# Kernel optimization log

Hardware: AMD Instinct MI355X
Metric: run time of the kernel (lower is better)

Reference implementation:

```python
import math
import jax, jax.numpy as jnp
import numpy as np

E_EDGES = 65536
N_NODES = 8192
MUL = 32
LAT = 128
COND = 32
# uuu tensor-product instructions (l1, l2, l_out) generated by the selection-rule loop
INSTR = [(0,0,0),(1,1,0),(2,2,0),
         (0,1,1),(1,0,1),(1,1,1),(1,2,1),(2,1,1),(2,2,1),
         (0,2,2),(1,1,2),(1,2,2),(2,0,2),(2,1,2),(2,2,2)]

# ---- real Wigner-3j (invariant 3-tensor) via null space of equivariance constraints ----
def _su2_J(l):
    m = np.arange(-l, l + 1)
    Jz = np.diag(m).astype(complex)
    d = 2 * l + 1
    Jp = np.zeros((d, d), complex)
    Jp[np.arange(1, d), np.arange(0, d - 1)] = np.sqrt((l - m[:-1]) * (l + m[:-1] + 1))
    Jm = Jp.conj().T
    return (Jp + Jm) / 2, (Jp - Jm) / 2j, Jz

def _q(l):
    q = np.zeros((2 * l + 1, 2 * l + 1), complex)
    for m in range(-l, 0):
        q[l + m, l + abs(m)] = 1 / np.sqrt(2)
        q[l + m, l - abs(m)] = -1j / np.sqrt(2)
    q[l, l] = 1.0
    for m in range(1, l + 1):
        q[l + m, l + abs(m)] = (-1) ** m / np.sqrt(2)
        q[l + m, l - abs(m)] = 1j * (-1) ** m / np.sqrt(2)
    return q

def _gen(l):
    q = _q(l)
    return [np.real(q.conj().T @ (-1j * J) @ q) for J in _su2_J(l)]

def _w3j(l1, l2, l3):
    G1, G2, G3 = _gen(l1), _gen(l2), _gen(l3)
    d1, d2, d3 = 2 * l1 + 1, 2 * l2 + 1, 2 * l3 + 1
    rows = []
    for a in range(3):
        rows.append(np.kron(np.kron(G1[a], np.eye(d2)), np.eye(d3))
                    + np.kron(np.kron(np.eye(d1), G2[a]), np.eye(d3))
                    + np.kron(np.kron(np.eye(d1), np.eye(d2)), G3[a]))
    _, _, vt = np.linalg.svd(np.concatenate(rows, 0))
    c = vt[-1]
    c = c / np.linalg.norm(c)
    c = c * np.sign(c[np.argmax(np.abs(c))])
    return c.reshape(d1, d2, d3).astype(np.float32)

W3J = {}
for _k in INSTR:
    if _k not in W3J:
        W3J[_k] = jnp.asarray(_w3j(*_k))

def _split9(x):
    # (E, MUL, 9) -> per-l blocks (widths 1,3,5)
    return (x[:, :, 0:1], x[:, :, 1:4], x[:, :, 4:9])

def _so3_ln(blocks, gamma, eps=1e-6):
    out = []
    for b, x in enumerate(blocks):
        if x.shape[-1] == 1:  # scalars: centered layernorm over channels
            mu = jnp.mean(x, axis=1, keepdims=True)
            var = jnp.mean((x - mu) ** 2, axis=1, keepdims=True)
            x = (x - mu) * jax.lax.rsqrt(var + eps)
        else:  # l>0: RMS over (channel, m), no centering (equivariance)
            ms = jnp.mean(x ** 2, axis=(1, 2), keepdims=True)
            x = x * jax.lax.rsqrt(ms + eps)
        out.append(x * gamma[b][None, :, None])
    return out

def _forward(scalar_latent, equiv_latent, edge_conditioning, update_coeff,
             W_env, b_env0, gamma_env, Wg_env, bg_env, gamma_tp,
             W1_s, b1_s, W2_s, b2_s, Weq0, beq0, Weq1, Weq2, Wg_eq, bg_eq,
             edge_index, active_edges):
    E = scalar_latent.shape[0]
    edge_center = edge_index[0]
    # env_eq: per-l SO3 linear (channel mixing), bias on l=0
    xb = _split9(equiv_latent)
    env = [jnp.einsum('eum,vu->evm', xb[l], W_env[l]) for l in range(3)]
    env[0] = env[0] + b_env0[None, :, None]
    gate_in = jnp.concatenate([scalar_latent, edge_conditioning], axis=-1)  # (E,160)
    g_env = 1.0 + 0.1 * jnp.tanh(gate_in @ Wg_env + bg_env[0])
    env_edges = jnp.concatenate(env, axis=-1) * g_env[:, None, None]
    # scatter-sum edges -> nodes, SO3 layernorm, gather back per edge
    env_nodes = jax.ops.segment_sum(env_edges, edge_center, num_segments=N_NODES)
    env_nodes = jnp.concatenate(_so3_ln(_split9(env_nodes), gamma_env), axis=-1)
    local = env_nodes[edge_center]  # (E, MUL, 9)
    # selection-rule-sparse tensor product, uuu, component-normalized
    x1b = _split9(equiv_latent)
    x2b = _split9(local)
    tp_blocks = [math.sqrt(2 * lo + 1) * jnp.einsum('ijk,eui,euj->euk', W3J[(l1, l2, lo)], x1b[l1], x2b[l2])
                 for (l1, l2, lo) in INSTR]
    tp_blocks = _so3_ln(tp_blocks, gamma_tp)
    # scalar (l=0) slices -> (E, 3*MUL)
    tp_scalars = jnp.concatenate(tp_blocks[0:3], axis=-1).reshape(E, -1)
    scalar_in = jnp.concatenate([tp_scalars, edge_conditioning], axis=-1)
    new_scalar = jax.nn.silu(scalar_in @ W1_s.T + b1_s) @ W2_s.T + b2_s  # (E, LAT)
    # equiv_update: SO3 linear tp_out_irreps -> equiv_latent_irreps
    x0 = tp_scalars  # (E, 3*MUL)
    out0 = (x0 @ Weq0.T + beq0)[:, :, None]                      # (E, MUL, 1)
    out1 = jnp.einsum('eum,vu->evm', jnp.concatenate(tp_blocks[3:9], axis=1), Weq1)   # (E, MUL, 3)
    out2 = jnp.einsum('eum,vu->evm', jnp.concatenate(tp_blocks[9:15], axis=1), Weq2)  # (E, MUL, 5)
    new_equiv = jnp.concatenate([out0, out1, out2], axis=-1)
    g_eq = 1.0 + 0.1 * jnp.tanh(gate_in @ Wg_eq + bg_eq[0])
    new_equiv = new_equiv * g_eq[:, None, None]
    # residual stream with update coefficient + index_add over active_edges
    c = update_coeff[0]
    co = jax.lax.rsqrt(c * c + 1.0)
    cn = c * co
    s_out = (co * scalar_latent).at[active_edges].add(cn * new_scalar)
    e_out = (co * equiv_latent).at[active_edges].add(cn * new_equiv)
    return s_out, e_out

def setup_inputs() -> dict:
    key = jax.random.key(0)
    ks = jax.random.split(key, 16)
    f32 = jnp.float32
    return {
        'scalar_latent': jax.random.normal(ks[0], (E_EDGES, LAT), f32),
        'equiv_latent': jax.random.normal(ks[1], (E_EDGES, MUL, 9), f32),
        'edge_conditioning': jax.random.normal(ks[2], (E_EDGES, COND), f32),
        'update_coeff': jnp.ones((1,), f32),
        'W_env': jax.random.normal(ks[3], (3, MUL, MUL), f32) / math.sqrt(MUL),
        'b_env0': jnp.zeros((MUL,), f32),
        'gamma_env': jnp.ones((3, MUL), f32),
        'Wg_env': jax.random.normal(ks[4], (LAT + COND,), f32) / math.sqrt(LAT + COND),
        'bg_env': jnp.zeros((1,), f32),
        'gamma_tp': jnp.ones((15, MUL), f32),
        'W1_s': jax.random.normal(ks[5], (LAT, 3 * MUL + COND), f32) / math.sqrt(3 * MUL + COND),
        'b1_s': jnp.zeros((LAT,), f32),
        'W2_s': jax.random.normal(ks[6], (LAT, LAT), f32) / math.sqrt(LAT),
        'b2_s': jnp.zeros((LAT,), f32),
        'Weq0': jax.random.normal(ks[7], (MUL, 3 * MUL), f32) / math.sqrt(3 * MUL),
        'beq0': jnp.zeros((MUL,), f32),
        'Weq1': jax.random.normal(ks[8], (MUL, 6 * MUL), f32) / math.sqrt(6 * MUL),
        'Weq2': jax.random.normal(ks[9], (MUL, 6 * MUL), f32) / math.sqrt(6 * MUL),
        'Wg_eq': jax.random.normal(ks[10], (LAT + COND,), f32) / math.sqrt(LAT + COND),
        'bg_eq': jnp.zeros((1,), f32),
        'edge_index': jax.random.randint(ks[11], (2, E_EDGES), 0, N_NODES),
        'active_edges': jnp.arange(E_EDGES),
    }

def reference(scalar_latent, equiv_latent, edge_conditioning, update_coeff,
              W_env, b_env0, gamma_env, Wg_env, bg_env, gamma_tp,
              W1_s, b1_s, W2_s, b2_s, Weq0, beq0, Weq1, Weq2, Wg_eq, bg_eq,
              edge_index, active_edges):
    return _forward(scalar_latent, equiv_latent, edge_conditioning, update_coeff,
                    W_env, b_env0, gamma_env, Wg_env, bg_env, gamma_tp,
                    W1_s, b1_s, W2_s, b2_s, Weq0, beq0, Weq1, Weq2, Wg_eq, bg_eq,
                    edge_index, active_edges)
```

## Files before the change

### kernel.cpp

```cpp
#include <hip/hip_runtime.h>
#include <math.h>

#define E_EDGES 65536
#define N_NODES 8192

typedef _Float16 half_t;
typedef _Float16 h8 __attribute__((ext_vector_type(8)));
typedef float f4 __attribute__((ext_vector_type(4)));

#define SSC_P 136

#define C3f   0.57735026918962576f
#define C5f   0.44721359549995794f
#define C10f  0.31622776601683794f
#define C30f  0.18257418583505536f
#define C30x2 0.36514837167011072f
#define A235  0.23904572186687872f
#define B370  0.20701966780270626f
#define C70f  0.11952286093343936f
#define S3f   1.7320508075688772f
#define S5f   2.2360679774997896f
#define S5n  -2.2360679774997896f


__device__ double factd(int n) { double r = 1.0; for (int i = 2; i <= n; ++i) r *= i; return r; }

__device__ double w3j_m(int j1, int j2, int j3, int m1, int m2, int m3) {
  if (m1 + m2 + m3 != 0) return 0.0;
  if (abs(m1) > j1 || abs(m2) > j2 || abs(m3) > j3) return 0.0;
  double delta = sqrt(factd(j1 + j2 - j3) * factd(j1 - j2 + j3) * factd(-j1 + j2 + j3)
                      / factd(j1 + j2 + j3 + 1));
  double pref = sqrt(factd(j1 + m1) * factd(j1 - m1) * factd(j2 + m2) * factd(j2 - m2)
                     * factd(j3 + m3) * factd(j3 - m3));
  int klo = max(0, max(j2 - j3 - m1, j1 + m2 - j3));
  int khi = min(j1 + j2 - j3, min(j1 - m1, j2 + m2));
  double s = 0.0;
  for (int k = klo; k <= khi; ++k) {
    double d = factd(k) * factd(j1 + j2 - j3 - k) * factd(j1 - m1 - k) * factd(j2 + m2 - k)
             * factd(j3 - j2 + m1 + k) * factd(j3 - j1 - m2 + k);
    s += ((k & 1) ? -1.0 : 1.0) / d;
  }
  int e = j1 - j2 - m3;
  double sg = ((e % 2 + 2) % 2) ? -1.0 : 1.0;
  return sg * delta * pref * s;
}

__device__ void qent(int l, int mr, int col, double* re, double* im) {
  const double v = 0.7071067811865475244;
  *re = 0.0; *im = 0.0;
  int m = mr - l;
  if (m < 0) {
    if (col == l - m) *re = v;
    else if (col == l + m) *im = -v;
  } else if (m == 0) {
    if (col == l) *re = 1.0;
  } else {
    double s = (m & 1) ? -1.0 : 1.0;
    if (col == l + m) *re = s * v;
    else if (col == l - m) *im = s * v;
  }
}

__constant__ const int GB_L1[15] = {0,1,2,0,1,1,1,2,2,0,1,1,2,2,2};
__constant__ const int GB_L2[15] = {0,1,2,1,0,1,2,1,2,2,1,2,0,1,2};
__constant__ const int GB_LO[15] = {0,0,0,1,1,1,1,1,1,2,2,2,2,2,2};
__constant__ const int GB_WOFF[15] = {0,1,10,35,44,53,80,125,170,245,270,315,390,415,490};
__constant__ const double GB_FLIP[15] = {1,1,1,1,1,-1,1,1,1,1,1,1,1,-1,-1};

extern "C" __global__ __launch_bounds__(128)
void gen_w3j(float* __restrict__ w3j_out) {
  __shared__ double vsh[128];
  __shared__ double red[128];
  __shared__ int redi[128];
  const int b = blockIdx.x;
  const int t = threadIdx.x;
  const int l1 = GB_L1[b], l2 = GB_L2[b], l3 = GB_LO[b];
  const int d1 = 2 * l1 + 1, d2 = 2 * l2 + 1, d3 = 2 * l3 + 1;
  const int n = d1 * d2 * d3;
  double tre = 0.0, tim = 0.0;
  if (t < n) {
    int a = t / (d2 * d3), r = t - a * (d2 * d3), bb = r / d3, c = r - bb * d3;
    for (int mr1 = 0; mr1 < d1; ++mr1) {
      double q1r, q1i; qent(l1, mr1, a, &q1r, &q1i); q1i = -q1i;
      if (q1r == 0.0 && q1i == 0.0) continue;
      int m1 = mr1 - l1;
      for (int mr2 = 0; mr2 < d2; ++mr2) {
        double q2r, q2i; qent(l2, mr2, bb, &q2r, &q2i); q2i = -q2i;
        if (q2r == 0.0 && q2i == 0.0) continue;
        int m2 = mr2 - l2;
        int m3 = -(m1 + m2);
        if (m3 < -l3 || m3 > l3) continue;
        double q3r, q3i; qent(l3, m3 + l3, c, &q3r, &q3i); q3i = -q3i;
        if (q3r == 0.0 && q3i == 0.0) continue;
        double w = w3j_m(l1, l2, l3, m1, m2, m3);
        if (w == 0.0) continue;
        double ar = q1r * q2r - q1i * q2i, ai = q1r * q2i + q1i * q2r;
        double cr = ar * q3r - ai * q3i, ci = ar * q3i + ai * q3r;
        tre += cr * w; tim += ci * w;
      }
    }
  }
  red[t] = tre * tre; __syncthreads();
  for (int s = 64; s; s >>= 1) { if (t < s) red[t] += red[t + s]; __syncthreads(); }
  double nre = red[0]; __syncthreads();
  red[t] = tim * tim; __syncthreads();
  for (int s = 64; s; s >>= 1) { if (t < s) red[t] += red[t + s]; __syncthreads(); }
  double nim = red[0]; __syncthreads();
  double v = (nre >= nim) ? tre : tim;
  v *= 1.0 / sqrt(nre >= nim ? nre : nim);
  red[t] = fabs(v); __syncthreads();
  for (int s = 64; s; s >>= 1) { if (t < s) red[t] = fmax(red[t], red[t + s]); __syncthreads(); }
  double mx = red[0]; __syncthreads();
  redi[t] = (t < n && fabs(v) >= mx * (1.0 - 1e-6)) ? t : 1 << 20; __syncthreads();
  for (int s = 64; s; s >>= 1) { if (t < s) redi[t] = min(redi[t], redi[t + s]); __syncthreads(); }
  int win = redi[0];
  vsh[t] = v; __syncthreads();
  double sgn = (vsh[win] < 0.0) ? -1.0 : 1.0;
  const double norm3[3] = {1.0, 1.7320508075688772, 2.2360679774997896};
  if (t < n) w3j_out[GB_WOFF[b] + t] = (float)(v * sgn * GB_FLIP[b] * norm3[l3]);
}

__device__ double gentry(int l, int axis, int a, int bcol) {
  int d = 2 * l + 1;
  double acc = 0.0;
  for (int m1 = 0; m1 < d; ++m1) {
    double q1r, q1i; qent(l, m1, a, &q1r, &q1i);
    if (q1r == 0.0 && q1i == 0.0) continue;
    for (int m2 = 0; m2 < d; ++m2) {
      double Jr = 0.0, Ji = 0.0;
      if (axis == 0) {
        if (m2 == m1 + 1) { double m = m1 - l; Jr = sqrt((l - m) * (l + m + 1)) * 0.5; }
        else if (m1 == m2 + 1) { double m = m2 - l; Jr = sqrt((l - m) * (l + m + 1)) * 0.5; }
      } else if (axis == 1) {
        if (m1 == m2 + 1) { double m = m2 - l; Ji = -sqrt((l - m) * (l + m + 1)) * 0.5; }
        else if (m2 == m1 + 1) { double m = m1 - l; Ji = sqrt((l - m) * (l + m + 1)) * 0.5; }
      } else {
        if (m1 == m2) Jr = m1 - l;
      }
      if (Jr == 0.0 && Ji == 0.0) continue;
      double Xr = Ji, Xi = -Jr;
      double q2r, q2i; qent(l, m2, bcol, &q2r, &q2i);
      if (q2r == 0.0 && q2i == 0.0) continue;
      double t1r = q1r * Xr + q1i * Xi;
      double t1i = q1r * Xi - q1i * Xr;
      acc += t1r * q2r - t1i * q2i;
    }
  }
  return acc;
}

extern "C" __global__ __launch_bounds__(128)
void check_w3j(const float* __restrict__ w3j_in, float* __restrict__ diag) {
  __shared__ double G1[3][5][5], G2[3][5][5], G3[3][5][5];
  __shared__ double c[125];
  __shared__ double red[128];
  const int b = blockIdx.x, t = threadIdx.x;
  const int l1 = GB_L1[b], l2 = GB_L2[b], l3 = GB_LO[b];
  const int d1 = 2 * l1 + 1, d2 = 2 * l2 + 1, d3 = 2 * l3 + 1;
  const int n = d1 * d2 * d3;
  const int n1 = d1 * d1, n2 = d2 * d2, n3 = d3 * d3;
  const int per = n1 + n2 + n3;
  for (int idx = t; idx < 3 * per; idx += 128) {
    int axis = idx / per, r = idx % per;
    int l, d; double* dst;
    if (r < n1)            { l = l1; d = d1; dst = &G1[axis][0][0]; }
    else if (r < n1 + n2)  { r -= n1; l = l2; d = d2; dst = &G2[axis][0][0]; }
    else                   { r -= n1 + n2; l = l3; d = d3; dst = &G3[axis][0][0]; }
    int a = r / d, bb2 = r % d;
    dst[a * 5 + bb2] = gentry(l, axis, a, bb2);
  }
  if (t < n) c[t] = (double)w3j_in[GB_WOFF[b] + t];
  __syncthreads();
  double rsq = 0.0, nsq = 0.0;
  if (t < n) {
    int i = t / (d2 * d3), j = (t / d3) % d2, k = t % d3;
    nsq = c[t] * c[t];
    for (int ax = 0; ax < 3; ++ax) {
      double acc = 0.0;
      for (int p = 0; p < d1; ++p) acc += G1[ax][i][p] * c[(p * d2 + j) * d3 + k];
      for (int p = 0; p < d2; ++p) acc += G2[ax][j][p] * c[(i * d2 + p) * d3 + k];
      for (int p = 0; p < d3; ++p) acc += G3[ax][k][p] * c[(i * d2 + j) * d3 + p];
      rsq += acc * acc;
    }
  }
  red[t] = rsq; __syncthreads();
  for (int s = 64; s; s >>= 1) { if (t < s) red[t] += red[t + s]; __syncthreads(); }
  double R = red[0]; __syncthreads();
  red[t] = nsq; __syncthreads();
  for (int s = 64; s; s >>= 1) { if (t < s) red[t] += red[t + s]; __syncthreads(); }
  if (t == 0) diag[b] = (float)(R / red[0]);
}

extern "C" __global__ void diag_fold(const float* __restrict__ diag, float* __restrict__ out_s) {
  if (blockIdx.x == 0 && threadIdx.x == 0) {
    int worst = -1; float wr = 0.f;
    for (int b = 0; b < 15; ++b) { float r = diag[b]; if (r > 1e-6f && r > wr) { wr = r; worst = b; } }
    if (worst >= 0) out_s[0] += 1000.f * (worst + 1) + 100.f * fminf(wr, 9.f);
  }
}

extern "C" __global__ __launch_bounds__(256)
void prep_weights(const float* __restrict__ W1, const float* __restrict__ W2,
                  const float* __restrict__ Weq0, const float* __restrict__ Weq1,
                  const float* __restrict__ Weq2,
                  half_t* __restrict__ W1F, half_t* __restrict__ W2F,
                  half_t* __restrict__ Weq0F, half_t* __restrict__ Weq1F,
                  half_t* __restrict__ Weq2F) {
  int t = blockIdx.x * blockDim.x + threadIdx.x;
  int stride = gridDim.x * blockDim.x;
  for (int f = t; f < 16384; f += stride) {
    int i = f & 7, lane = (f >> 3) & 63, ks = (f >> 9) & 3, nt = f >> 11;
    int n = nt * 16 + (lane & 15);
    int k = ks * 32 + (lane >> 4) * 8 + i;
    W1F[f] = (half_t)W1[n * 128 + k];
    W2F[f] = (half_t)W2[n * 128 + k];
  }
  for (int f = t; f < 3072; f += stride) {
    int i = f & 7, lane = (f >> 3) & 63, rest = f >> 9;
    int ks = rest % 3, nt = rest / 3;
    int n = nt * 16 + (lane & 15);
    int k = ks * 32 + (lane >> 4) * 8 + i;
    Weq0F[f] = (half_t)Weq0[n * 96 + k];
  }
  for (int f = t; f < 6144; f += stride) {
    int i = f & 7, lane = (f >> 3) & 63, rest = f >> 9;
    int ks = rest % 6, nt = rest / 6;
    int n = nt * 16 + (lane & 15);
    int k = ks * 32 + (lane >> 4) * 8 + i;
    Weq1F[f] = (half_t)Weq1[n * 192 + k];
    Weq2F[f] = (half_t)Weq2[n * 192 + k];
  }
}

extern "C" __global__ __launch_bounds__(256)
void gate_count(const float* __restrict__ scalar, const float* __restrict__ cond,
                const float* __restrict__ Wg_env, const float* __restrict__ bg_env,
                const float* __restrict__ Wg_eq, const float* __restrict__ bg_eq,
                const int* __restrict__ edge_index,
                float* __restrict__ g_env, float* __restrict__ g_eq,
                int* __restrict__ counts) {
  const int t = threadIdx.x;
  const int e0 = blockIdx.x * 8;
  const int eg = t >> 5, lane = t & 31;
  size_t e = (size_t)(e0 + eg);
  float pa = 0.f, pb = 0.f;
  for (int i = lane; i < 160; i += 32) {
    float xi = (i < 128) ? scalar[e * 128 + i] : cond[e * 32 + (i - 128)];
    pa = fmaf(xi, Wg_env[i], pa);
    pb = fmaf(xi, Wg_eq[i], pb);
  }
  for (int off = 16; off; off >>= 1) { pa += __shfl_xor(pa, off); pb += __shfl_xor(pb, off); }
  if (lane == 0) {
    g_env[e] = 1.f + 0.1f * tanhf(pa + bg_env[0]);
    g_eq[e]  = 1.f + 0.1f * tanhf(pb + bg_eq[0]);
  }
  if (t < 8) atomicAdd(&counts[edge_index[e0 + t]], 1);
}

extern "C" __global__ __launch_bounds__(256)
void csr_scan(int* __restrict__ counts, int* __restrict__ offsets) {
  __shared__ int part[256];
  __shared__ int pre[257];
  const int t = threadIdx.x;
  const int base = t * 32;
  int s = 0;
  for (int i = 0; i < 32; ++i) s += counts[base + i];
  part[t] = s; __syncthreads();
  if (t == 0) { int a = 0; for (int i = 0; i < 256; ++i) { pre[i] = a; a += part[i]; } pre[256] = a; }
  __syncthreads();
  int run = pre[t];
  for (int i = 0; i < 32; ++i) {
    int c = counts[base + i];
    offsets[base + i] = run;
    counts[base + i] = run;
    run += c;
  }
  if (t == 0) offsets[N_NODES] = pre[256];
}

extern "C" __global__ __launch_bounds__(256)
void csr_fill(const int* __restrict__ edge_index, int* __restrict__ cursor,
              int* __restrict__ elist) {
  int e = blockIdx.x * 256 + threadIdx.x;
  if (e < E_EDGES) {
    int pos = atomicAdd(&cursor[edge_index[e]], 1);
    elist[pos] = e;
  }
}

extern "C" __global__ __launch_bounds__(64)
void env_build(const float* __restrict__ equiv, const float* __restrict__ g_env,
               const int* __restrict__ elist, const int* __restrict__ offsets,
               const float* __restrict__ W_env, const float* __restrict__ b_env0,
               const float* __restrict__ gamma_env, float* __restrict__ env_nodes) {
  __shared__ float xs[288];
  const int n = blockIdx.x, t = threadIdx.x;
  const int lo = offsets[n], hi = offsets[n + 1];
  float acc0 = 0.f, acc1 = 0.f, acc2 = 0.f, acc3 = 0.f, acc4 = 0.f, gsum = 0.f;
  for (int idx = lo; idx < hi; ++idx) {
    int e = elist[idx];
    float g = g_env[e];
    gsum += g;
    const float* row = equiv + (size_t)e * 288;
    acc0 = fmaf(g, row[t], acc0);
    acc1 = fmaf(g, row[t + 64], acc1);
    acc2 = fmaf(g, row[t + 128], acc2);
    acc3 = fmaf(g, row[t + 192], acc3);
    if (t < 32) acc4 = fmaf(g, row[t + 256], acc4);
  }
  xs[t] = acc0; xs[t + 64] = acc1; xs[t + 128] = acc2; xs[t + 192] = acc3;
  if (t < 32) xs[t + 256] = acc4;
  __syncthreads();
  float ev[9];
  if (t < 32) {
    const int v = t;
#pragma unroll
    for (int m = 0; m < 9; ++m) {
      int l = (m == 0) ? 0 : (m < 4 ? 1 : 2);
      const float4* Wr = (const float4*)(W_env + (size_t)(l * 32 + v) * 32);
      float s = 0.f;
#pragma unroll
      for (int u4 = 0; u4 < 8; ++u4) {
        float4 wv = Wr[u4];
        int ub = u4 * 4;
        s = fmaf(wv.x, xs[(ub + 0) * 9 + m], s);
        s = fmaf(wv.y, xs[(ub + 1) * 9 + m], s);
        s = fmaf(wv.z, xs[(ub + 2) * 9 + m], s);
        s = fmaf(wv.w, xs[(ub + 3) * 9 + m], s);
      }
      if (m == 0) s += b_env0[v] * gsum;
      ev[m] = s;
    }
    float s0 = ev[0], q0 = ev[0] * ev[0];
#pragma unroll
    for (int off = 16; off; off >>= 1) { s0 += __shfl_xor(s0, off); q0 += __shfl_xor(q0, off); }
    float mean0 = s0 * (1.f / 32.f);
    float var0 = q0 * (1.f / 32.f) - mean0 * mean0;
    float r0 = rsqrtf(var0 + 1e-6f);
    float q1 = ev[1] * ev[1] + ev[2] * ev[2] + ev[3] * ev[3];
#pragma unroll
    for (int off = 16; off; off >>= 1) q1 += __shfl_xor(q1, off);
    float r1 = rsqrtf(q1 * (1.f / 96.f) + 1e-6f);
    float q2 = ev[4]*ev[4] + ev[5]*ev[5] + ev[6]*ev[6] + ev[7]*ev[7] + ev[8]*ev[8];
#pragma unroll
    for (int off = 16; off; off >>= 1) q2 += __shfl_xor(q2, off);
    float r2 = rsqrtf(q2 * (1.f / 160.f) + 1e-6f);
    ev[0] = (ev[0] - mean0) * r0 * gamma_env[v];
    float g1 = r1 * gamma_env[32 + v], g2 = r2 * gamma_env[64 + v];
    ev[1] *= g1; ev[2] *= g1; ev[3] *= g1;
    ev[4] *= g2; ev[5] *= g2; ev[6] *= g2; ev[7] *= g2; ev[8] *= g2;
  }
  __syncthreads();
  if (t < 32) {
#pragma unroll
    for (int m = 0; m < 9; ++m) xs[t * 9 + m] = ev[m];
  }
  __syncthreads();
  float* outb = env_nodes + (size_t)n * 288;
  outb[t] = xs[t]; outb[t + 64] = xs[t + 64];
  outb[t + 128] = xs[t + 128]; outb[t + 192] = xs[t + 192];
  if (t < 32) outb[t + 256] = xs[t + 256];
}

extern "C" __global__ __launch_bounds__(512, 4)
void edge_update(const float* __restrict__ scalar, const float* __restrict__ equiv,
                 const float* __restrict__ cond, const float* __restrict__ updc,
                 const float* __restrict__ env_nodes, const float* __restrict__ gamma_tp,
                 const half_t* __restrict__ W1F, const float* __restrict__ b1,
                 const half_t* __restrict__ W2F, const float* __restrict__ b2,
                 const half_t* __restrict__ Weq0F, const float* __restrict__ beq0,
                 const half_t* __restrict__ Weq1F, const half_t* __restrict__ Weq2F,
                 const float* __restrict__ g_eq,
                 const int* __restrict__ edge_index, const int* __restrict__ active_edges,
                 const float* __restrict__ w3j, float* __restrict__ out_s,
                 float* __restrict__ out_e) {
  __shared__ __align__(16) half_t stp[48 * 16 * 32];
  __shared__ __align__(16) half_t ssc[16 * SSC_P];
  __shared__ __align__(16) half_t shh[16 * SSC_P];
  __shared__ float sg[16];
  __shared__ int snode[16];
  __shared__ int sact[16];
  const int t = threadIdx.x;
  const int e0 = blockIdx.x * 16;
  const float cc = updc[0];
  const float co = rsqrtf(cc * cc + 1.f);
  const float cn = cc * co;

  if (t < 16) {
    snode[t] = edge_index[e0 + t];
    sact[t] = active_edges[e0 + t];
    sg[t] = g_eq[e0 + t];
  }
  {
    int e = t >> 5, j = t & 31;
    ssc[e * SSC_P + 96 + j] = (half_t)cond[(size_t)(e0 + e) * 32 + j];
  }
  __syncthreads();

  {
    const int eg = t >> 5, u = t & 31;
    const float* arow = equiv + (size_t)(e0 + eg) * 288 + u * 9;
    const float* brow = env_nodes + (size_t)snode[eg] * 288 + u * 9;
    float a0 = arow[0], b0 = brow[0];
    float A1[3] = {arow[1], arow[2], arow[3]};
    float A2[5] = {arow[4], arow[5], arow[6], arow[7], arow[8]};
    float B1[3] = {brow[1], brow[2], brow[3]};
    float B2[5] = {brow[4], brow[5], brow[6], brow[7], brow[8]};
    float o[51];
    o[0] = a0 * b0;
    o[1] = C3f * (A1[0]*B1[0] + A1[1]*B1[1] + A1[2]*B1[2]);
    o[2] = C5f * (A2[0]*B2[0] + A2[1]*B2[1] + A2[2]*B2[2] + A2[3]*B2[3] + A2[4]*B2[4]);
    o[3] = a0 * B1[0]; o[4] = a0 * B1[1]; o[5] = a0 * B1[2];
    o[6] = A1[0] * b0; o[7] = A1[1] * b0; o[8] = A1[2] * b0;
    o[9] = o[10] = o[11] = 0.f;
#pragma unroll
    for (int i = 0; i < 3; ++i)
#pragma unroll
      for (int j = 0; j < 3; ++j) {
        float p = A1[i] * B1[j];
#pragma unroll
        for (int k = 0; k < 3; ++k)
          o[9 + k] = fmaf(w3j[53 + (i * 3 + j) * 3 + k], p, o[9 + k]);
      }
    o[12] = S3f * (C10f*(A1[1]*B2[1] + A1[2]*B2[0]) - C30f*A1[0]*B2[2] - C10f*A1[0]*B2[4]);
    o[13] = S3f * (C10f*(A1[0]*B2[1] + A1[2]*B2[3]) + C30x2*A1[1]*B2[2]);
    o[14] = S3f * (C10f*(A1[0]*B2[0] + A1[1]*B2[3] + A1[2]*B2[4]) - C30f*A1[2]*B2[2]);
    o[15] = S3f * (C10f*(A2[1]*B1[1] + A2[0]*B1[2]) - C30f*A2[2]*B1[0] - C10f*A2[4]*B1[0]);
    o[16] = S3f * (C10f*(A2[1]*B1[0] + A2[3]*B1[2]) + C30x2*A2[2]*B1[1]);
    o[17] = S3f * (C10f*(A2[0]*B1[0] + A2[3]*B1[1] + A2[4]*B1[2]) - C30f*A2[2]*B1[2]);
    o[18] = o[19] = o[20] = 0.f;
#pragma unroll
    for (int i = 0; i < 5; ++i)
#pragma unroll
      for (int j = 0; j < 5; ++j) {
        float p = A2[i] * B2[j];
#pragma unroll
        for (int k = 0; k < 3; ++k)
          o[18 + k] = fmaf(w3j[170 + (i * 5 + j) * 3 + k], p, o[18 + k]);
      }
    o[21] = a0 * B2[0]; o[22] = a0 * B2[1]; o[23] = a0 * B2[2]; o[24] = a0 * B2[3]; o[25] = a0 * B2[4];
    o[26] = S5f * C10f * (A1[2]*B1[0] + A1[0]*B1[2]);
    o[27] = S5f * C10f * (A1[0]*B1[1] + A1[1]*B1[0]);
    o[28] = S5f * (C30x2*A1[1]*B1[1] - C30f*(A1[0]*B1[0] + A1[2]*B1[2]));
    o[29] = S5f * C10f * (A1[1]*B1[2] + A1[2]*B1[1]);
    o[30] = S5f * C10f * (A1[2]*B1[2] - A1[0]*B1[0]);
    o[31] = S5f * (C30f*(A1[2]*B2[3] - A1[0]*B2[1]) - C30x2*A1[1]*B2[4]);
    o[32] = S5f * (C30f*(A1[0]*B2[0] - A1[1]*B2[3] + A1[2]*B2[4]) + C10f*A1[2]*B2[2]);
    o[33] = S5f * C10f * (A1[0]*B2[3] - A1[2]*B2[1]);
    o[34] = S5f * (C30f*(A1[1]*B2[1] - A1[2]*B2[0] + A1[0]*B2[4]) - C10f*A1[0]*B2[2]);
    o[35] = S5f * (C30x2*A1[1]*B2[0] - C30f*(A1[2]*B2[1] + A1[0]*B2[3]));
    o[36] = A2[0] * b0; o[37] = A2[1] * b0; o[38] = A2[2] * b0; o[39] = A2[3] * b0; o[40] = A2[4] * b0;
    o[41] = S5n * (C30f*(A2[3]*B1[2] - A2[1]*B1[0]) - C30x2*A2[4]*B1[1]);
    o[42] = S5n * (C30f*(A2[0]*B1[0] - A2[3]*B1[1] + A2[4]*B1[2]) + C10f*A2[2]*B1[2]);
    o[43] = S5n * C10f * (A2[3]*B1[0] - A2[1]*B1[2]);
    o[44] = S5n * (C30f*(A2[1]*B1[1] - A2[0]*B1[2] + A2[4]*B1[0]) - C10f*A2[2]*B1[0]);
    o[45] = S5n * (C30x2*A2[0]*B1[1] - C30f*(A2[1]*B1[2] + A2[3]*B1[0]));
    o[46] = S5n * (A235*(A2[0]*B2[2] + A2[2]*B2[0]) - B370*(A2[1]*B2[3] + A2[3]*B2[1]));
    o[47] = S5n * (-B370*(A2[0]*B2[3] + A2[3]*B2[0]) - C70f*(A2[1]*B2[2] + A2[2]*B2[1]) + B370*(A2[1]*B2[4] + A2[4]*B2[1]));
    o[48] = S5n * (A235*(A2[0]*B2[0] - A2[2]*B2[2] + A2[4]*B2[4]) - C70f*(A2[1]*B2[1] + A2[3]*B2[3]));
    o[49] = S5n * (-B370*(A2[0]*B2[1] + A2[1]*B2[0]) - C70f*(A2[3]*B2[2] + A2[2]*B2[3]) - B370*(A2[3]*B2[4] + A2[4]*B2[3]));
    o[50] = S5n * (B370*(A2[1]*B2[1] - A2[3]*B2[3]) + A235*(A2[2]*B2[4] + A2[4]*B2[2]));

#pragma unroll
    for (int b = 0; b < 3; ++b) {
      float x = o[b];
      float s = x, q = x * x;
#pragma unroll
      for (int off = 16; off; off >>= 1) { s += __shfl_xor(s, off); q += __shfl_xor(q, off); }
      float mean = s * (1.f / 32.f);
      float var = q * (1.f / 32.f) - mean * mean;
      ssc[eg * SSC_P + u * 3 + b] = (half_t)((x - mean) * rsqrtf(var + 1e-6f) * gamma_tp[b * 32 + u]);
    }
    const int offs[12] = {3, 6, 9, 12, 15, 18, 21, 26, 31, 36, 41, 46};
    const int d3s[12]  = {3, 3, 3, 3, 3, 3, 5, 5, 5, 5, 5, 5};
    const int uswz = u ^ ((eg & 3) << 3);
#pragma unroll
    for (int bb = 0; bb < 12; ++bb) {
      float q = 0.f;
#pragma unroll
      for (int k = 0; k < d3s[bb]; ++k) { float x = o[offs[bb] + k]; q += x * x; }
#pragma unroll
      for (int off = 16; off; off >>= 1) q += __shfl_xor(q, off);
      float scale = rsqrtf(q / (32.f * d3s[bb]) + 1e-6f) * gamma_tp[(bb + 3) * 32 + u];
#pragma unroll
      for (int k = 0; k < d3s[bb]; ++k)
        stp[((offs[bb] + k - 3) * 16 + eg) * 32 + uswz] = (half_t)(o[offs[bb] + k] * scale);
    }
  }
  __syncthreads();

  const int l = t & 63, wave = t >> 6;
  const int g = l >> 4, c = l & 15;
  f4 mlp2acc;

  {
    const int nt = wave;
    float bn = b1[nt * 16 + c];
    f4 acc = {bn, bn, bn, bn};
#pragma unroll
    for (int ks = 0; ks < 4; ++ks) {
      h8 a = *(const h8*)&ssc[c * SSC_P + ks * 32 + g * 8];
      h8 b = *(const h8*)&W1F[(((nt * 4 + ks) * 64) + l) * 8];
      acc = __builtin_amdgcn_mfma_f32_16x16x32_f16(a, b, acc, 0, 0, 0);
    }
#pragma unroll
    for (int i = 0; i < 4; ++i) {
      float x = acc[i];
      shh[(4 * g + i) * SSC_P + nt * 16 + c] = (half_t)(x / (1.f + expf(-x)));
    }
  }
  __syncthreads();

  {
    const int nt = wave;
    float bn = b2[nt * 16 + c];
    f4 acc = {bn, bn, bn, bn};
#pragma unroll
    for (int ks = 0; ks < 4; ++ks) {
      h8 a = *(const h8*)&shh[c * SSC_P + ks * 32 + g * 8];
      h8 b = *(const h8*)&W2F[(((nt * 4 + ks) * 64) + l) * 8];
      acc = __builtin_amdgcn_mfma_f32_16x16x32_f16(a, b, acc, 0, 0, 0);
    }
    mlp2acc = acc;
  }

  f4 accT[3];
  int nTiles = 0;
  for (int T = wave; T < 18; T += 8, ++nTiles) {
    f4 acc;
    if (T < 2) {
      const int nt = T;
      float bv = beq0[nt * 16 + c];
      acc = (f4){bv, bv, bv, bv};
#pragma unroll
      for (int ks = 0; ks < 3; ++ks) {
        h8 a = *(const h8*)&ssc[c * SSC_P + ks * 32 + g * 8];
        h8 b = *(const h8*)&Weq0F[(((nt * 3 + ks) * 64) + l) * 8];
        acc = __builtin_amdgcn_mfma_f32_16x16x32_f16(a, b, acc, 0, 0, 0);
      }
    } else if (T < 8) {
      const int idx = T - 2, Mt = idx >> 1, nt = idx & 1;
      const int row = Mt * 16 + c;
      const int e = row / 3, m = row - e * 3;
      const int gx = (g ^ (e & 3)) * 8;
      acc = (f4){0.f, 0.f, 0.f, 0.f};
#pragma unroll
      for (int ks = 0; ks < 6; ++ks) {
        int kk = ks * 3 + m;
        h8 a = *(const h8*)&stp[(kk * 16 + e) * 32 + gx];
        h8 b = *(const h8*)&Weq1F[(((nt * 6 + ks) * 64) + l) * 8];
        acc = __builtin_amdgcn_mfma_f32_16x16x32_f16(a, b, acc, 0, 0, 0);
      }
    } else {
      const int idx = T - 8, Mt = idx >> 1, nt = idx & 1;
      const int row = Mt * 16 + c;
      const int e = row / 5, m = row - e * 5;
      const int gx = (g ^ (e & 3)) * 8;
      acc = (f4){0.f, 0.f, 0.f, 0.f};
#pragma unroll
      for (int ks = 0; ks < 6; ++ks) {
        int kk = 18 + ks * 5 + m;
        h8 a = *(const h8*)&stp[(kk * 16 + e) * 32 + gx];
        h8 b = *(const h8*)&Weq2F[(((nt * 6 + ks) * 64) + l) * 8];
        acc = __builtin_amdgcn_mfma_f32_16x16x32_f16(a, b, acc, 0, 0, 0);
      }
    }
    accT[nTiles] = acc;
  }
  __syncthreads();

  {
    float* tmp  = reinterpret_cast<float*>(&stp[0]);
    float* sout = tmp + 4608;
    int slot = 0;
    for (int T = wave; T < 18; T += 8, ++slot) {
      f4 acc = accT[slot];
      int Mt, nt, type;
      if (T < 2)      { type = 0; Mt = 0; nt = T; }
      else if (T < 8) { type = 1; Mt = (T - 2) >> 1; nt = (T - 2) & 1; }
      else            { type = 2; Mt = (T - 8) >> 1; nt = (T - 8) & 1; }
      const int v = nt * 16 + c;
#pragma unroll
      for (int i = 0; i < 4; ++i) {
        int row = Mt * 16 + 4 * g + i;
        int e, off;
        if (type == 0)      { e = row; off = 0; }
        else if (type == 1) { e = row / 3; off = 1 + (row - e * 3); }
        else                { e = row / 5; off = 4 + (row - e * 5); }
        tmp[e * 288 + v * 9 + off] = cn * sg[e] * acc[i];
      }
    }
    {
      const int nt = wave;
#pragma unroll
      for (int i = 0; i < 4; ++i)
        sout[(4 * g + i) * 128 + nt * 16 + c] = cn * mlp2acc[i];
    }
  }
  __syncthreads();

  {
    const float* tmp  = reinterpret_cast<const float*>(&stp[0]);
    const float* sout = tmp + 4608;
    const float4* tmp4 = (const float4*)tmp;
    for (int i = t; i < 16 * 72; i += 512) {
      int e = i / 72, q = i - e * 72;
      size_t r = (size_t)sact[e];
      const float4 ev = *(const float4*)&equiv[r * 288 + q * 4];
      float4 tv = tmp4[i];
      float4 ov;
      ov.x = co * ev.x + tv.x; ov.y = co * ev.y + tv.y;
      ov.z = co * ev.z + tv.z; ov.w = co * ev.w + tv.w;
      *(float4*)&out_e[r * 288 + q * 4] = ov;
    }
    for (int i = t; i < 16 * 128; i += 512) {
      int e = i >> 7, n = i & 127;
      size_t r = (size_t)sact[e];
      out_s[r * 128 + n] = co * scalar[r * 128 + n] + sout[i];
    }
  }
}

extern "C" void kernel_launch(void* const* d_in, const int* in_sizes, int n_in,
                              void* d_out, int out_size, void* d_ws, size_t ws_size,
                              hipStream_t stream) {
  const float* scalar     = (const float*)d_in[0];
  const float* equiv      = (const float*)d_in[1];
  const float* cond       = (const float*)d_in[2];
  const float* updc       = (const float*)d_in[3];
  const float* W_env      = (const float*)d_in[4];
  const float* b_env0     = (const float*)d_in[5];
  const float* gamma_env  = (const float*)d_in[6];
  const float* Wg_env     = (const float*)d_in[7];
  const float* bg_env     = (const float*)d_in[8];
  const float* gamma_tp   = (const float*)d_in[9];
  const float* W1         = (const float*)d_in[10];
  const float* b1         = (const float*)d_in[11];
  const float* W2         = (const float*)d_in[12];
  const float* b2         = (const float*)d_in[13];
  const float* Weq0       = (const float*)d_in[14];
  const float* beq0       = (const float*)d_in[15];
  const float* Weq1       = (const float*)d_in[16];
  const float* Weq2       = (const float*)d_in[17];
  const float* Wg_eq      = (const float*)d_in[18];
  const float* bg_eq      = (const float*)d_in[19];
  const int* edge_index   = (const int*)d_in[20];
  const int* active_edges = (const int*)d_in[21];

  float* out_s = (float*)d_out;
  float* out_e = out_s + (size_t)E_EDGES * 128;

  float* ws    = (float*)d_ws;
  float* env   = ws;
  float* w3jt  = env + (size_t)N_NODES * 288;
  float* diag  = w3jt + 640;
  half_t* W1F   = (half_t*)(diag + 16);
  half_t* W2F   = W1F + 16384;
  half_t* Weq0F = W2F + 16384;
  half_t* Weq1F = Weq0F + 3072;
  half_t* Weq2F = Weq1F + 6144;
  int* counts  = (int*)(Weq2F + 6144);
  int* offsets = counts + N_NODES;
  float* g_eq  = (float*)(offsets + N_NODES + 1);
  float* g_env = out_s + ((size_t)E_EDGES * (128 + 288) - 131072);
  int* elist   = (int*)(g_env + 65536);

  hipMemsetAsync(counts, 0, N_NODES * sizeof(int), stream);
  gen_w3j<<<15, 128, 0, stream>>>(w3jt);
  check_w3j<<<15, 128, 0, stream>>>(w3jt, diag);
  prep_weights<<<48, 256, 0, stream>>>(W1, W2, Weq0, Weq1, Weq2,
                                       W1F, W2F, Weq0F, Weq1F, Weq2F);
  gate_count<<<E_EDGES / 8, 256, 0, stream>>>(scalar, cond, Wg_env, bg_env, Wg_eq, bg_eq,
                                              edge_index, g_env, g_eq, counts);
  csr_scan<<<1, 256, 0, stream>>>(counts, offsets);
  csr_fill<<<E_EDGES / 256, 256, 0, stream>>>(edge_index, counts, elist);
  env_build<<<N_NODES, 64, 0, stream>>>(equiv, g_env, elist, offsets,
                                        W_env, b_env0, gamma_env, env);
  edge_update<<<E_EDGES / 16, 512, 0, stream>>>(scalar, equiv, cond, updc, env, gamma_tp,
                                                W1F, b1, W2F, b2, Weq0F, beq0, Weq1F, Weq2F,
                                                g_eq, edge_index, active_edges,
                                                w3jt, out_s, out_e);
  diag_fold<<<1, 64, 0, stream>>>(diag, out_s);
}
```

Measured before the change: 242.9 us.

## Drop w3j self-check kernels, widen env_build, pack two edges per TP thread

Removes the check_w3j and diag_fold diagnostic kernels, which validated the generated Wigner-3j tensors and folded an error code into the output. env_build now runs 128 threads per node instead of 64, so each thread accumulates fewer strided columns. In edge_update, only half the threads compute the tensor product, each handling two edges with float2 vector math so packed FP32 ops can be used, while the other half sit idle in that phase. Dropping the check saves two small launches but also removes a correctness safeguard.

```diff
diff --git a/kernel.cpp b/kernel.cpp
--- a/kernel.cpp
+++ b/kernel.cpp
@@ -7,6 +7,7 @@
 typedef _Float16 half_t;
 typedef _Float16 h8 __attribute__((ext_vector_type(8)));
 typedef float f4 __attribute__((ext_vector_type(4)));
+typedef float f2 __attribute__((ext_vector_type(2)));
 
 #define SSC_P 136
 
@@ -120,85 +121,6 @@
   if (t < n) w3j_out[GB_WOFF[b] + t] = (float)(v * sgn * GB_FLIP[b] * norm3[l3]);
 }
 
-__device__ double gentry(int l, int axis, int a, int bcol) {
-  int d = 2 * l + 1;
-  double acc = 0.0;
-  for (int m1 = 0; m1 < d; ++m1) {
-    double q1r, q1i; qent(l, m1, a, &q1r, &q1i);
-    if (q1r == 0.0 && q1i == 0.0) continue;
-    for (int m2 = 0; m2 < d; ++m2) {
-      double Jr = 0.0, Ji = 0.0;
-      if (axis == 0) {
-        if (m2 == m1 + 1) { double m = m1 - l; Jr = sqrt((l - m) * (l + m + 1)) * 0.5; }
-        else if (m1 == m2 + 1) { double m = m2 - l; Jr = sqrt((l - m) * (l + m + 1)) * 0.5; }
-      } else if (axis == 1) {
-        if (m1 == m2 + 1) { double m = m2 - l; Ji = -sqrt((l - m) * (l + m + 1)) * 0.5; }
-        else if (m2 == m1 + 1) { double m = m1 - l; Ji = sqrt((l - m) * (l + m + 1)) * 0.5; }
-      } else {
-        if (m1 == m2) Jr = m1 - l;
-      }
-      if (Jr == 0.0 && Ji == 0.0) continue;
-      double Xr = Ji, Xi = -Jr;
-      double q2r, q2i; qent(l, m2, bcol, &q2r, &q2i);
-      if (q2r == 0.0 && q2i == 0.0) continue;
-      double t1r = q1r * Xr + q1i * Xi;
-      double t1i = q1r * Xi - q1i * Xr;
-      acc += t1r * q2r - t1i * q2i;
-    }
-  }
-  return acc;
-}
-
-extern "C" __global__ __launch_bounds__(128)
-void check_w3j(const float* __restrict__ w3j_in, float* __restrict__ diag) {
-  __shared__ double G1[3][5][5], G2[3][5][5], G3[3][5][5];
-  __shared__ double c[125];
-  __shared__ double red[128];
-  const int b = blockIdx.x, t = threadIdx.x;
-  const int l1 = GB_L1[b], l2 = GB_L2[b], l3 = GB_LO[b];
-  const int d1 = 2 * l1 + 1, d2 = 2 * l2 + 1, d3 = 2 * l3 + 1;
-  const int n = d1 * d2 * d3;
-  const int n1 = d1 * d1, n2 = d2 * d2, n3 = d3 * d3;
-  const int per = n1 + n2 + n3;
-  for (int idx = t; idx < 3 * per; idx += 128) {
-    int axis = idx / per, r = idx % per;
-    int l, d; double* dst;
-    if (r < n1)            { l = l1; d = d1; dst = &G1[axis][0][0]; }
-    else if (r < n1 + n2)  { r -= n1; l = l2; d = d2; dst = &G2[axis][0][0]; }
-    else                   { r -= n1 + n2; l = l3; d = d3; dst = &G3[axis][0][0]; }
-    int a = r / d, bb2 = r % d;
-    dst[a * 5 + bb2] = gentry(l, axis, a, bb2);
-  }
-  if (t < n) c[t] = (double)w3j_in[GB_WOFF[b] + t];
-  __syncthreads();
-  double rsq = 0.0, nsq = 0.0;
-  if (t < n) {
-    int i = t / (d2 * d3), j = (t / d3) % d2, k = t % d3;
-    nsq = c[t] * c[t];
-    for (int ax = 0; ax < 3; ++ax) {
-      double acc = 0.0;
-      for (int p = 0; p < d1; ++p) acc += G1[ax][i][p] * c[(p * d2 + j) * d3 + k];
-      for (int p = 0; p < d2; ++p) acc += G2[ax][j][p] * c[(i * d2 + p) * d3 + k];
-      for (int p = 0; p < d3; ++p) acc += G3[ax][k][p] * c[(i * d2 + j) * d3 + p];
-      rsq += acc * acc;
-    }
-  }
-  red[t] = rsq; __syncthreads();
-  for (int s = 64; s; s >>= 1) { if (t < s) red[t] += red[t + s]; __syncthreads(); }
-  double R = red[0]; __syncthreads();
-  red[t] = nsq; __syncthreads();
-  for (int s = 64; s; s >>= 1) { if (t < s) red[t] += red[t + s]; __syncthreads(); }
-  if (t == 0) diag[b] = (float)(R / red[0]);
-}
-
-extern "C" __global__ void diag_fold(const float* __restrict__ diag, float* __restrict__ out_s) {
-  if (blockIdx.x == 0 && threadIdx.x == 0) {
-    int worst = -1; float wr = 0.f;
-    for (int b = 0; b < 15; ++b) { float r = diag[b]; if (r > 1e-6f && r > wr) { wr = r; worst = b; } }
-    if (worst >= 0) out_s[0] += 1000.f * (worst + 1) + 100.f * fminf(wr, 9.f);
-  }
-}
-
 extern "C" __global__ __launch_bounds__(256)
 void prep_weights(const float* __restrict__ W1, const float* __restrict__ W2,
                   const float* __restrict__ Weq0, const float* __restrict__ Weq1,
@@ -288,7 +210,7 @@
   }
 }
 
-extern "C" __global__ __launch_bounds__(64)
+extern "C" __global__ __launch_bounds__(128)
 void env_build(const float* __restrict__ equiv, const float* __restrict__ g_env,
                const int* __restrict__ elist, const int* __restrict__ offsets,
                const float* __restrict__ W_env, const float* __restrict__ b_env0,
@@ -296,20 +218,18 @@
   __shared__ float xs[288];
   const int n = blockIdx.x, t = threadIdx.x;
   const int lo = offsets[n], hi = offsets[n + 1];
-  float acc0 = 0.f, acc1 = 0.f, acc2 = 0.f, acc3 = 0.f, acc4 = 0.f, gsum = 0.f;
+  float acc0 = 0.f, acc1 = 0.f, acc2 = 0.f, gsum = 0.f;
   for (int idx = lo; idx < hi; ++idx) {
     int e = elist[idx];
     float g = g_env[e];
     gsum += g;
     const float* row = equiv + (size_t)e * 288;
     acc0 = fmaf(g, row[t], acc0);
-    acc1 = fmaf(g, row[t + 64], acc1);
-    acc2 = fmaf(g, row[t + 128], acc2);
-    acc3 = fmaf(g, row[t + 192], acc3);
-    if (t < 32) acc4 = fmaf(g, row[t + 256], acc4);
-  }
-  xs[t] = acc0; xs[t + 64] = acc1; xs[t + 128] = acc2; xs[t + 192] = acc3;
-  if (t < 32) xs[t + 256] = acc4;
+    acc1 = fmaf(g, row[t + 128], acc1);
+    if (t < 32) acc2 = fmaf(g, row[t + 256], acc2);
+  }
+  xs[t] = acc0; xs[t + 128] = acc1;
+  if (t < 32) xs[t + 256] = acc2;
   __syncthreads();
   float ev[9];
   if (t < 32) {
@@ -357,9 +277,12 @@
   }
   __syncthreads();
   float* outb = env_nodes + (size_t)n * 288;
-  outb[t] = xs[t]; outb[t + 64] = xs[t + 64];
-  outb[t + 128] = xs[t + 128]; outb[t + 192] = xs[t + 192];
+  outb[t] = xs[t]; outb[t + 128] = xs[t + 128];
   if (t < 32) outb[t + 256] = xs[t + 256];
+}
+
+__device__ inline f2 shfl_xor2(f2 v, int off) {
+  f2 r; r.x = __shfl_xor(v.x, off); r.y = __shfl_xor(v.y, off); return r;
 }
 
 extern "C" __global__ __launch_bounds__(512, 4)
@@ -397,30 +320,33 @@
   }
   __syncthreads();
 
-  {
+  if (t < 256) {
     const int eg = t >> 5, u = t & 31;
-    const float* arow = equiv + (size_t)(e0 + eg) * 288 + u * 9;
-    const float* brow = env_nodes + (size_t)snode[eg] * 288 + u * 9;
-    float a0 = arow[0], b0 = brow[0];
-    float A1[3] = {arow[1], arow[2], arow[3]};
-    float A2[5] = {arow[4], arow[5], arow[6], arow[7], arow[8]};
-    float B1[3] = {brow[1], brow[2], brow[3]};
-    float B2[5] = {brow[4], brow[5], brow[6], brow[7], brow[8]};
-    float o[51];
+    const float* aA = equiv + (size_t)(e0 + eg) * 288 + u * 9;
+    const float* aB = equiv + (size_t)(e0 + eg + 8) * 288 + u * 9;
+    const float* bA = env_nodes + (size_t)snode[eg] * 288 + u * 9;
+    const float* bB = env_nodes + (size_t)snode[eg + 8] * 288 + u * 9;
+    f2 a0 = {aA[0], aB[0]}, b0 = {bA[0], bB[0]};
+    f2 A1[3], B1[3], A2[5], B2[5];
+#pragma unroll
+    for (int i = 0; i < 3; ++i) { A1[i] = (f2){aA[1 + i], aB[1 + i]}; B1[i] = (f2){bA[1 + i], bB[1 + i]}; }
+#pragma unroll
+    for (int i = 0; i < 5; ++i) { A2[i] = (f2){aA[4 + i], aB[4 + i]}; B2[i] = (f2){bA[4 + i], bB[4 + i]}; }
+    f2 o[51];
     o[0] = a0 * b0;
     o[1] = C3f * (A1[0]*B1[0] + A1[1]*B1[1] + A1[2]*B1[2]);
     o[2] = C5f * (A2[0]*B2[0] + A2[1]*B2[1] + A2[2]*B2[2] + A2[3]*B2[3] + A2[4]*B2[4]);
     o[3] = a0 * B1[0]; o[4] = a0 * B1[1]; o[5] = a0 * B1[2];
     o[6] = A1[0] * b0; o[7] = A1[1] * b0; o[8] = A1[2] * b0;
-    o[9] = o[10] = o[11] = 0.f;
+    o[9] = o[10] = o[11] = (f2){0.f, 0.f};
 #pragma unroll
     for (int i = 0; i < 3; ++i)
 #pragma unroll
       for (int j = 0; j < 3; ++j) {
-        float p = A1[i] * B1[j];
+        f2 p = A1[i] * B1[j];
 #pragma unroll
         for (int k = 0; k < 3; ++k)
-          o[9 + k] = fmaf(w3j[53 + (i * 3 + j) * 3 + k], p, o[9 + k]);
+          o[9 + k] += w3j[53 + (i * 3 + j) * 3 + k] * p;
       }
     o[12] = S3f * (C10f*(A1[1]*B2[1] + A1[2]*B2[0]) - C30f*A1[0]*B2[2] - C10f*A1[0]*B2[4]);
     o[13] = S3f * (C10f*(A1[0]*B2[1] + A1[2]*B2[3]) + C30x2*A1[1]*B2[2]);
@@ -428,31 +354,31 @@
     o[15] = S3f * (C10f*(A2[1]*B1[1] + A2[0]*B1[2]) - C30f*A2[2]*B1[0] - C10f*A2[4]*B1[0]);
     o[16] = S3f * (C10f*(A2[1]*B1[0] + A2[3]*B1[2]) + C30x2*A2[2]*B1[1]);
     o[17] = S3f * (C10f*(A2[0]*B1[0] + A2[3]*B1[1] + A2[4]*B1[2]) - C30f*A2[2]*B1[2]);
-    o[18] = o[19] = o[20] = 0.f;
+    o[18] = o[19] = o[20] = (f2){0.f, 0.f};
 #pragma unroll
     for (int i = 0; i < 5; ++i)
 #pragma unroll
       for (int j = 0; j < 5; ++j) {
-        float p = A2[i] * B2[j];
+        f2 p = A2[i] * B2[j];
 #pragma unroll
         for (int k = 0; k < 3; ++k)
-          o[18 + k] = fmaf(w3j[170 + (i * 5 + j) * 3 + k], p, o[18 + k]);
+          o[18 + k] += w3j[170 + (i * 5 + j) * 3 + k] * p;
       }
     o[21] = a0 * B2[0]; o[22] = a0 * B2[1]; o[23] = a0 * B2[2]; o[24] = a0 * B2[3]; o[25] = a0 * B2[4];
-    o[26] = S5f * C10f * (A1[2]*B1[0] + A1[0]*B1[2]);
-    o[27] = S5f * C10f * (A1[0]*B1[1] + A1[1]*B1[0]);
+    o[26] = (S5f * C10f) * (A1[2]*B1[0] + A1[0]*B1[2]);
+    o[27] = (S5f * C10f) * (A1[0]*B1[1] + A1[1]*B1[0]);
     o[28] = S5f * (C30x2*A1[1]*B1[1] - C30f*(A1[0]*B1[0] + A1[2]*B1[2]));
-    o[29] = S5f * C10f * (A1[1]*B1[2] + A1[2]*B1[1]);
-    o[30] = S5f * C10f * (A1[2]*B1[2] - A1[0]*B1[0]);
+    o[29] = (S5f * C10f) * (A1[1]*B1[2] + A1[2]*B1[1]);
+    o[30] = (S5f * C10f) * (A1[2]*B1[2] - A1[0]*B1[0]);
     o[31] = S5f * (C30f*(A1[2]*B2[3] - A1[0]*B2[1]) - C30x2*A1[1]*B2[4]);
     o[32] = S5f * (C30f*(A1[0]*B2[0] - A1[1]*B2[3] + A1[2]*B2[4]) + C10f*A1[2]*B2[2]);
-    o[33] = S5f * C10f * (A1[0]*B2[3] - A1[2]*B2[1]);
+    o[33] = (S5f * C10f) * (A1[0]*B2[3] - A1[2]*B2[1]);
     o[34] = S5f * (C30f*(A1[1]*B2[1] - A1[2]*B2[0] + A1[0]*B2[4]) - C10f*A1[0]*B2[2]);
     o[35] = S5f * (C30x2*A1[1]*B2[0] - C30f*(A1[2]*B2[1] + A1[0]*B2[3]));
     o[36] = A2[0] * b0; o[37] = A2[1] * b0; o[38] = A2[2] * b0; o[39] = A2[3] * b0; o[40] = A2[4] * b0;
     o[41] = S5n * (C30f*(A2[3]*B1[2] - A2[1]*B1[0]) - C30x2*A2[4]*B1[1]);
     o[42] = S5n * (C30f*(A2[0]*B1[0] - A2[3]*B1[1] + A2[4]*B1[2]) + C10f*A2[2]*B1[2]);
-    o[43] = S5n * C10f * (A2[3]*B1[0] - A2[1]*B1[2]);
+    o[43] = (S5n * C10f) * (A2[3]*B1[0] - A2[1]*B1[2]);
     o[44] = S5n * (C30f*(A2[1]*B1[1] - A2[0]*B1[2] + A2[4]*B1[0]) - C10f*A2[2]*B1[0]);
     o[45] = S5n * (C30x2*A2[0]*B1[1] - C30f*(A2[1]*B1[2] + A2[3]*B1[0]));
     o[46] = S5n * (A235*(A2[0]*B2[2] + A2[2]*B2[0]) - B370*(A2[1]*B2[3] + A2[3]*B2[1]));
@@ -463,28 +389,37 @@
 
 #pragma unroll
     for (int b = 0; b < 3; ++b) {
-      float x = o[b];
-      float s = x, q = x * x;
-#pragma unroll
-      for (int off = 16; off; off >>= 1) { s += __shfl_xor(s, off); q += __shfl_xor(q, off); }
-      float mean = s * (1.f / 32.f);
-      float var = q * (1.f / 32.f) - mean * mean;
-      ssc[eg * SSC_P + u * 3 + b] = (half_t)((x - mean) * rsqrtf(var + 1e-6f) * gamma_tp[b * 32 + u]);
+      f2 x = o[b];
+      f2 s = x, q = x * x;
+#pragma unroll
+      for (int off = 16; off; off >>= 1) { s += shfl_xor2(s, off); q += shfl_xor2(q, off); }
+      f2 mean = s * (1.f / 32.f);
+      f2 var = q * (1.f / 32.f) - mean * mean;
+      f2 r = {rsqrtf(var.x + 1e-6f), rsqrtf(var.y + 1e-6f)};
+      float gt = gamma_tp[b * 32 + u];
+      f2 y = (x - mean) * r * gt;
+      ssc[eg * SSC_P + u * 3 + b] = (half_t)y.x;
+      ssc[(eg + 8) * SSC_P + u * 3 + b] = (half_t)y.y;
     }
     const int offs[12] = {3, 6, 9, 12, 15, 18, 21, 26, 31, 36, 41, 46};
     const int d3s[12]  = {3, 3, 3, 3, 3, 3, 5, 5, 5, 5, 5, 5};
     const int uswz = u ^ ((eg & 3) << 3);
 #pragma unroll
     for (int bb = 0; bb < 12; ++bb) {
-      float q = 0.f;
-#pragma unroll
-      for (int k = 0; k < d3s[bb]; ++k) { float x = o[offs[bb] + k]; q += x * x; }
-#pragma unroll
-      for (int off = 16; off; off >>= 1) q += __shfl_xor(q, off);
-      float scale = rsqrtf(q / (32.f * d3s[bb]) + 1e-6f) * gamma_tp[(bb + 3) * 32 + u];
-#pragma unroll
-      for (int k = 0; k < d3s[bb]; ++k)
-        stp[((offs[bb] + k - 3) * 16 + eg) * 32 + uswz] = (half_t)(o[offs[bb] + k] * scale);
+      f2 q = {0.f, 0.f};
+#pragma unroll
+      for (int k = 0; k < d3s[bb]; ++k) { f2 x = o[offs[bb] + k]; q += x * x; }
+#pragma unroll
+      for (int off = 16; off; off >>= 1) q += shfl_xor2(q, off);
+      float gt = gamma_tp[(bb + 3) * 32 + u];
+      f2 scale = {rsqrtf(q.x / (32.f * d3s[bb]) + 1e-6f) * gt,
+                  rsqrtf(q.y / (32.f * d3s[bb]) + 1e-6f) * gt};
+#pragma unroll
+      for (int k = 0; k < d3s[bb]; ++k) {
+        f2 y = o[offs[bb] + k] * scale;
+        stp[((offs[bb] + k - 3) * 16 + eg) * 32 + uswz] = (half_t)y.x;
+        stp[((offs[bb] + k - 3) * 16 + eg + 8) * 32 + uswz] = (half_t)y.y;
+      }
     }
   }
   __syncthreads();
@@ -667,18 +602,16 @@
 
   hipMemsetAsync(counts, 0, N_NODES * sizeof(int), stream);
   gen_w3j<<<15, 128, 0, stream>>>(w3jt);
-  check_w3j<<<15, 128, 0, stream>>>(w3jt, diag);
   prep_weights<<<48, 256, 0, stream>>>(W1, W2, Weq0, Weq1, Weq2,
                                        W1F, W2F, Weq0F, Weq1F, Weq2F);
   gate_count<<<E_EDGES / 8, 256, 0, stream>>>(scalar, cond, Wg_env, bg_env, Wg_eq, bg_eq,
                                               edge_index, g_env, g_eq, counts);
   csr_scan<<<1, 256, 0, stream>>>(counts, offsets);
   csr_fill<<<E_EDGES / 256, 256, 0, stream>>>(edge_index, counts, elist);
-  env_build<<<N_NODES, 64, 0, stream>>>(equiv, g_env, elist, offsets,
-                                        W_env, b_env0, gamma_env, env);
+  env_build<<<N_NODES, 128, 0, stream>>>(equiv, g_env, elist, offsets,
+                                         W_env, b_env0, gamma_env, env);
   edge_update<<<E_EDGES / 16, 512, 0, stream>>>(scalar, equiv, cond, updc, env, gamma_tp,
                                                 W1F, b1, W2F, b2, Weq0F, beq0, Weq1F, Weq2F,
                                                 g_eq, edge_index, active_edges,
                                                 w3jt, out_s, out_e);
-  diag_fold<<<1, 64, 0, stream>>>(diag, out_s);
-}
+}
```

New measurement: 270.2 us. +11.2%, slower.
